# Kernel tuning notes

Hardware: AMD Instinct MI355X
Metric: run time of the kernel (lower is better)

## Reference

```python
import jax, jax.numpy as jnp
import numpy as np

H = 8          # nhead
EPS_Z = 1e-6   # linear-attention normalizer eps
LN_EPS = 1e-5  # torch LayerNorm default


def _ln(x, g, b):
    m = x.mean(-1, keepdims=True)
    v = ((x - m) ** 2).mean(-1, keepdims=True)
    return (x - m) * jax.lax.rsqrt(v + LN_EPS) * g + b


def setup_inputs() -> dict:
    key = jax.random.key(0)
    ks = jax.random.split(key, 8)
    B, S, E, F = 4, 8192, 512, 2048
    s = 0.02
    return {
        "src": jax.random.normal(ks[0], (B, S, E), jnp.float32),
        "Wq": jax.random.normal(ks[1], (E, E), jnp.float32) * s,
        "bq": jnp.zeros((E,), jnp.float32),
        "Wk": jax.random.normal(ks[2], (E, E), jnp.float32) * s,
        "bk": jnp.zeros((E,), jnp.float32),
        "Wv": jax.random.normal(ks[3], (E, E), jnp.float32) * s,
        "bv": jnp.zeros((E,), jnp.float32),
        "Wo": jax.random.normal(ks[4], (E, E), jnp.float32) * s,
        "bo": jnp.zeros((E,), jnp.float32),
        "W1": jax.random.normal(ks[5], (E, F), jnp.float32) * s,
        "b1": jnp.zeros((F,), jnp.float32),
        "W2": jax.random.normal(ks[6], (F, E), jnp.float32) * s,
        "b2": jnp.zeros((E,), jnp.float32),
        "g1": jnp.ones((E,), jnp.float32),
        "be1": jnp.zeros((E,), jnp.float32),
        "g2": jnp.ones((E,), jnp.float32),
        "be2": jnp.zeros((E,), jnp.float32),
    }


def reference(src, Wq, bq, Wk, bk, Wv, bv, Wo, bo, W1, b1, W2, b2, g1, be1, g2, be2):
    B, S, E = src.shape
    Dh = E // H

    def heads(x):  # [B,S,E] -> [B,H,S,Dh]
        return x.reshape(B, S, H, Dh).transpose(0, 2, 1, 3)

    q = heads(src @ Wq + bq)
    k = heads(src @ Wk + bk)
    v = heads(src @ Wv + bv)

    qm = jax.nn.elu(q) + 1.0  # feature map: ELU+1
    km = jax.nn.elu(k) + 1.0

    kv = jnp.einsum("bhsd,bhse->bhde", km, v)          # [B,H,Dh,Dh]
    ksum = km.sum(axis=2)                               # [B,H,Dh]
    z = 1.0 / (jnp.einsum("bhsd,bhd->bhs", qm, ksum) + EPS_Z)
    attn = jnp.einsum("bhsd,bhde->bhse", qm, kv) * z[..., None]

    attn = attn.transpose(0, 2, 1, 3).reshape(B, S, E) @ Wo + bo
    x = _ln(src + attn, g1, be1)
    ff = jax.nn.relu(x @ W1 + b1) @ W2 + b2
    return _ln(x + ff, g2, be2)
```

## Files before the change

kernel.cpp:

```cpp
#include <hip/hip_runtime.h>
#include <hip/hip_bf16.h>

typedef __attribute__((ext_vector_type(8))) short bf16x8;
typedef __attribute__((ext_vector_type(4))) float f32x4;

__device__ inline ushort f2bf(float f) {
    uint u = __float_as_uint(f);
    u += 0x7fff + ((u >> 16) & 1);
    return (ushort)(u >> 16);
}
__device__ inline float bf2f(ushort h) {
    return __uint_as_float(((uint)h) << 16);
}

__device__ inline void gload16(const void* g, void* lds) {
    __builtin_amdgcn_global_load_lds(
        (const __attribute__((address_space(1))) void*)g,
        (__attribute__((address_space(3))) void*)lds, 16, 0, 0);
}

__global__ void conv_bf16(const float* __restrict__ in, ushort* __restrict__ out, int n4) {
    int i = blockIdx.x * 256 + threadIdx.x;
    if (i >= n4) return;
    float4 a = ((const float4*)in)[i];
    ushort4 o;
    o.x = f2bf(a.x); o.y = f2bf(a.y); o.z = f2bf(a.z); o.w = f2bf(a.w);
    ((ushort4*)out)[i] = o;
}

__global__ void wconv_t(const float* __restrict__ in, ushort* __restrict__ out, int K, int N) {
    __shared__ float tile[32][33];
    int kb = blockIdx.y * 32, nb = blockIdx.x * 32;
    int tx = threadIdx.x & 31, ty = threadIdx.x >> 5;
#pragma unroll
    for (int i = 0; i < 4; i++)
        tile[ty + i * 8][tx] = in[(size_t)(kb + ty + i * 8) * N + nb + tx];
    __syncthreads();
#pragma unroll
    for (int i = 0; i < 4; i++) {
        int n = nb + ty + i * 8, k = kb + tx;
        out[(size_t)n * K + k] = f2bf(tile[tx][ty + i * 8]);
    }
}

__global__ void biascat(const float* __restrict__ a, const float* __restrict__ b,
                        const float* __restrict__ c, float* __restrict__ o) {
    int i = blockIdx.x * 256 + threadIdx.x;
    if (i < 512) o[i] = a[i];
    else if (i < 1024) o[i] = b[i - 512];
    else if (i < 1536) o[i] = c[i - 1024];
}

template <int EPI, int NT>
__global__ __launch_bounds__(512, 2) void gemm256(
    const ushort* __restrict__ A, const ushort* __restrict__ Bt,
    const float* __restrict__ bias, const ushort* __restrict__ res16,
    ushort* __restrict__ out16, int M, int N, int K, int nbxg) {
    extern __shared__ char smem[];
    const int t = threadIdx.x;
    const int w = t >> 6, l = t & 63;
    const int wr = w >> 2, wc = w & 3;
    const int nwg = gridDim.x;
    const int cpx = nwg >> 3;
    const int swz = (blockIdx.x & 7) * cpx + (blockIdx.x >> 3);
    const int bxg = swz % nbxg, by = swz / nbxg;
    const int bx0 = bxg * NT;

    const int sc = (t & 3) ^ ((t >> 3) & 3);
    const ushort* gA0 = A + (size_t)(by * 256 + (t >> 2)) * K + sc * 8;
    const ushort* gA1 = gA0 + (size_t)128 * K;
    const ushort* sB0 = Bt + (size_t)(bx0 * 256 + (t >> 2)) * K + sc * 8;
    const ushort* sB1 = sB0 + (size_t)128 * K;

    const int Kt = K >> 5;
    const int TOT = NT * Kt;
    int stg_kt = 0, stg_g = 0;

    auto stage_h0 = [&]() {
        char* Lb = smem + (stg_g & 3) * 32768 + (w << 10);
        gload16(gA0 + stg_kt * 32, Lb);
        gload16(sB0 + stg_kt * 32, Lb + 16384);
    };
    auto stage_h1 = [&]() {
        char* Lb = smem + (stg_g & 3) * 32768 + (w << 10);
        gload16(gA1 + stg_kt * 32, Lb + 8192);
        gload16(sB1 + stg_kt * 32, Lb + 24576);
        ++stg_g;
        if (++stg_kt == Kt) {
            stg_kt = 0;
            sB0 += (size_t)256 * K;
            sB1 += (size_t)256 * K;
        }
    };

    f32x4 acc[8][4] = {};

    const int R0a = wr * 128 + (l & 15);
    const int offA = R0a * 64 + (((l >> 4) ^ ((R0a >> 1) & 3)) << 4);
    const int R0b = wc * 64 + (l & 15);
    const int offB = 16384 + R0b * 64 + (((l >> 4) ^ ((R0b >> 1) & 3)) << 4);

    stage_h0(); stage_h1();
    stage_h0(); stage_h1();
    stage_h0(); stage_h1();

    int g = 0;
    for (int j = 0; j < NT; ++j) {
#pragma unroll 1
        for (int kt = 0; kt < Kt; ++kt, ++g) {
            const int rem = TOT - 1 - g;
            if (rem >= 2)      asm volatile("s_waitcnt vmcnt(8)" ::: "memory");
            else if (rem == 1) asm volatile("s_waitcnt vmcnt(4)" ::: "memory");
            else               asm volatile("s_waitcnt vmcnt(0)" ::: "memory");
            __builtin_amdgcn_s_barrier();
            __builtin_amdgcn_sched_barrier(0);

            const char* bufp = smem + (g & 3) * 32768;
            bf16x8 a[8], b[4];
            b[0] = *(const bf16x8*)(bufp + offB);
            b[1] = *(const bf16x8*)(bufp + offB + 1024);
            b[2] = *(const bf16x8*)(bufp + offB + 2048);
            b[3] = *(const bf16x8*)(bufp + offB + 3072);
            a[0] = *(const bf16x8*)(bufp + offA);
            a[1] = *(const bf16x8*)(bufp + offA + 1024);
            a[2] = *(const bf16x8*)(bufp + offA + 2048);
            a[3] = *(const bf16x8*)(bufp + offA + 3072);
            if (g + 3 < TOT) stage_h0();
            __builtin_amdgcn_sched_barrier(0);
            __builtin_amdgcn_s_barrier();
            asm volatile("s_waitcnt lgkmcnt(0)" ::: "memory");
            __builtin_amdgcn_sched_barrier(0);
            __builtin_amdgcn_s_setprio(1);
#pragma unroll
            for (int m = 0; m < 4; m++)
#pragma unroll
                for (int n = 0; n < 4; n++)
                    acc[m][n] = __builtin_amdgcn_mfma_f32_16x16x32_bf16(a[m], b[n], acc[m][n], 0, 0, 0);
            __builtin_amdgcn_s_setprio(0);
            __builtin_amdgcn_sched_barrier(0);
            a[4] = *(const bf16x8*)(bufp + offA + 4096);
            a[5] = *(const bf16x8*)(bufp + offA + 5120);
            a[6] = *(const bf16x8*)(bufp + offA + 6144);
            a[7] = *(const bf16x8*)(bufp + offA + 7168);
            if (g + 3 < TOT) stage_h1();
            __builtin_amdgcn_sched_barrier(0);
            __builtin_amdgcn_s_barrier();
            asm volatile("s_waitcnt lgkmcnt(0)" ::: "memory");
            __builtin_amdgcn_sched_barrier(0);
            __builtin_amdgcn_s_setprio(1);
#pragma unroll
            for (int m = 4; m < 8; m++)
#pragma unroll
                for (int n = 0; n < 4; n++)
                    acc[m][n] = __builtin_amdgcn_mfma_f32_16x16x32_bf16(a[m], b[n], acc[m][n], 0, 0, 0);
            __builtin_amdgcn_s_setprio(0);
            __builtin_amdgcn_sched_barrier(0);
        }

        {
            const int bx = bx0 + j;
            const int row0 = by * 256 + wr * 128 + ((l >> 4) << 2);
            const int col0 = bx * 256 + wc * 64 + (l & 15);
            const int seg = bx >> 1;
            const size_t segoff = (size_t)seg * M * 512;
            const int c511 = col0 & 511;
            float bv[4];
#pragma unroll
            for (int n = 0; n < 4; n++) bv[n] = bias[col0 + n * 16];
#pragma unroll
            for (int m = 0; m < 8; m++) {
#pragma unroll
                for (int r = 0; r < 4; r++) {
                    const int row = row0 + m * 16 + r;
                    const size_t base = (size_t)row * N + col0;
#pragma unroll
                    for (int n = 0; n < 4; n++) {
                        float vv = acc[m][n][r] + bv[n];
                        if constexpr (EPI == 2) {
                            vv = vv > 0.f ? vv : 0.f;
                            out16[base + n * 16] = f2bf(vv);
                        } else if constexpr (EPI == 3) {
                            vv += bf2f(res16[base + n * 16]);
                            out16[base + n * 16] = f2bf(vv);
                        } else if constexpr (EPI == 4) {
                            if (seg < 2) vv = vv > 0.f ? vv + 1.f : __expf(vv);
                            out16[segoff + (size_t)row * 512 + c511 + n * 16] = f2bf(vv);
                        } else {
                            out16[base + n * 16] = f2bf(vv);
                        }
                    }
                }
            }
            if (j + 1 < NT) {
#pragma unroll
                for (int m = 0; m < 8; m++)
#pragma unroll
                    for (int n = 0; n < 4; n++)
                        acc[m][n] = (f32x4){0.f, 0.f, 0.f, 0.f};
            }
        }
    }
}

__global__ __launch_bounds__(256) void kv_partial(
    const ushort* __restrict__ km, const ushort* __restrict__ v,
    float* __restrict__ kvp, float* __restrict__ ksump, int S) {
    __shared__ ushort kms[32 * 64];
    __shared__ ushort vs[32 * 64];
    const int t = threadIdx.x;
    const int bh = blockIdx.y, b = bh >> 3, h = bh & 7;
    const int d0 = (t >> 4) * 4, e0 = (t & 15) * 4;
    float acc[4][4] = {};
    float ks = 0.f;
    const int s_base = blockIdx.x * 512;
    const int r = t >> 3, c8 = (t & 7) * 8;
    for (int s0 = 0; s0 < 512; s0 += 32) {
        size_t grow = ((size_t)b * S + s_base + s0 + r) * 512 + h * 64 + c8;
        *(uint4*)&kms[r * 64 + c8] = *(const uint4*)&km[grow];
        *(uint4*)&vs[r * 64 + c8] = *(const uint4*)&v[grow];
        __syncthreads();
#pragma unroll 4
        for (int s = 0; s < 32; ++s) {
            ushort4 ka = *(const ushort4*)&kms[s * 64 + d0];
            ushort4 vb = *(const ushort4*)&vs[s * 64 + e0];
            float a0 = bf2f(ka.x), a1 = bf2f(ka.y), a2 = bf2f(ka.z), a3 = bf2f(ka.w);
            float b0 = bf2f(vb.x), b1 = bf2f(vb.y), b2 = bf2f(vb.z), b3 = bf2f(vb.w);
            acc[0][0] += a0 * b0; acc[0][1] += a0 * b1; acc[0][2] += a0 * b2; acc[0][3] += a0 * b3;
            acc[1][0] += a1 * b0; acc[1][1] += a1 * b1; acc[1][2] += a1 * b2; acc[1][3] += a1 * b3;
            acc[2][0] += a2 * b0; acc[2][1] += a2 * b1; acc[2][2] += a2 * b2; acc[2][3] += a2 * b3;
            acc[3][0] += a3 * b0; acc[3][1] += a3 * b1; acc[3][2] += a3 * b2; acc[3][3] += a3 * b3;
            if (t < 64) ks += bf2f(kms[s * 64 + t]);
        }
        __syncthreads();
    }
    float* dst = kvp + ((size_t)bh * 16 + blockIdx.x) * 4096;
#pragma unroll
    for (int i = 0; i < 4; i++)
#pragma unroll
        for (int j = 0; j < 4; j++)
            dst[(d0 + i) * 64 + e0 + j] = acc[i][j];
    if (t < 64) ksump[((size_t)bh * 16 + blockIdx.x) * 64 + t] = ks;
}

__global__ void kv_reduce(const float* __restrict__ kvp, const float* __restrict__ ksump,
                          ushort* __restrict__ kvt, float* __restrict__ ksum) {
    int i = blockIdx.x * 256 + threadIdx.x;
    if (i < 32 * 4096) {
        int bh = i >> 12, de = i & 4095;
        int d = de >> 6, e = de & 63;
        float s = 0.f;
#pragma unroll
        for (int c = 0; c < 16; ++c) s += kvp[((size_t)bh * 16 + c) * 4096 + de];
        kvt[(size_t)bh * 4096 + e * 64 + d] = f2bf(s);
    } else {
        int j = i - 32 * 4096;
        if (j < 32 * 64) {
            int bh = j >> 6, d = j & 63;
            float s = 0.f;
#pragma unroll
            for (int c = 0; c < 16; ++c) s += ksump[((size_t)bh * 16 + c) * 64 + d];
            ksum[j] = s;
        }
    }
}

__global__ __launch_bounds__(256) void attn_mfma(
    const ushort* __restrict__ qm, const ushort* __restrict__ kvt,
    const float* __restrict__ ksum, ushort* __restrict__ attnE, int S) {
    __shared__ ushort As[128 * 128];
    __shared__ ushort Bs[128 * 64];
    __shared__ float zbuf[128][2];
    __shared__ float ks2[128];
    const int t = threadIdx.x, w = t >> 6, l = t & 63;
    const int cx = blockIdx.x, by = blockIdx.y;
    const int b = (by * 128) / S;
    const int h0 = cx * 2;
    const size_t arow0 = (size_t)(by * 128) * 512 + cx * 128;

#pragma unroll
    for (int rd = 0; rd < 8; ++rd) {
        const ushort* g = qm + arow0 + (size_t)(rd * 16 + w * 4 + (l >> 4)) * 512 + (l & 15) * 8;
        gload16(g, (char*)As + rd * 4096 + w * 1024);
    }
    const ushort* kvbase = kvt + (size_t)(b * 8 + h0) * 4096;
#pragma unroll
    for (int rd = 0; rd < 4; ++rd) {
        const ushort* g = kvbase + (rd * 32 + w * 8 + (l >> 3)) * 64 + (l & 7) * 8;
        gload16(g, (char*)Bs + rd * 4096 + w * 1024);
    }
    if (t < 128) ks2[t] = ksum[(b * 8 + h0) * 64 + t];
    __syncthreads();

    {
        const int r = t >> 1, hh = t & 1;
        float den = 0.f;
#pragma unroll
        for (int d0 = 0; d0 < 64; d0 += 8) {
            bf16x8 qv = *(const bf16x8*)&As[r * 128 + hh * 64 + d0];
#pragma unroll
            for (int j = 0; j < 8; j++) den += bf2f((ushort)qv[j]) * ks2[hh * 64 + d0 + j];
        }
        zbuf[r][hh] = 1.0f / (den + 1e-6f);
    }

    const int wr = w >> 1, wc = w & 1;
    const int ar = wr * 64 + (l & 15);
    const int br = wc * 64 + (l & 15);
    const int ko = (l >> 4) * 8;
    f32x4 acc[4][4] = {};
#pragma unroll
    for (int ks_ = 0; ks_ < 2; ++ks_) {
        bf16x8 a[4], bb[4];
#pragma unroll
        for (int m = 0; m < 4; m++)
            a[m] = *(const bf16x8*)&As[(ar + m * 16) * 128 + wc * 64 + ks_ * 32 + ko];
#pragma unroll
        for (int n = 0; n < 4; n++)
            bb[n] = *(const bf16x8*)&Bs[(br + n * 16) * 64 + ks_ * 32 + ko];
#pragma unroll
        for (int m = 0; m < 4; m++)
#pragma unroll
            for (int n = 0; n < 4; n++)
                acc[m][n] = __builtin_amdgcn_mfma_f32_16x16x32_bf16(a[m], bb[n], acc[m][n], 0, 0, 0);
    }
    __syncthreads();

    const int row0l = wr * 64 + ((l >> 4) << 2);
    ushort* outbase = attnE + (size_t)(by * 128) * 512 + cx * 128;
#pragma unroll
    for (int n = 0; n < 4; n++) {
#pragma unroll
        for (int m = 0; m < 4; m++) {
#pragma unroll
            for (int r = 0; r < 4; r++) {
                int rl = row0l + m * 16 + r;
                float z = zbuf[rl][wc];
                outbase[(size_t)rl * 512 + wc * 64 + n * 16 + (l & 15)] = f2bf(acc[m][n][r] * z);
            }
        }
    }
}

template <int OUT32>
__global__ __launch_bounds__(256) void ln_bf16(
    const ushort* __restrict__ in, const float* __restrict__ g, const float* __restrict__ be,
    void* __restrict__ outp, int Mrows) {
    const int w = threadIdx.x >> 6, l = threadIdx.x & 63;
    const int row = blockIdx.x * 4 + w;
    if (row >= Mrows) return;
    const ushort* rp = in + (size_t)row * 512;
    uint4 u = *(const uint4*)&rp[l * 8];
    float x[8];
    x[0] = bf2f((ushort)(u.x & 0xffff)); x[1] = bf2f((ushort)(u.x >> 16));
    x[2] = bf2f((ushort)(u.y & 0xffff)); x[3] = bf2f((ushort)(u.y >> 16));
    x[4] = bf2f((ushort)(u.z & 0xffff)); x[5] = bf2f((ushort)(u.z >> 16));
    x[6] = bf2f((ushort)(u.w & 0xffff)); x[7] = bf2f((ushort)(u.w >> 16));
    float s = 0.f, ss = 0.f;
#pragma unroll
    for (int j = 0; j < 8; j++) { s += x[j]; ss += x[j] * x[j]; }
#pragma unroll
    for (int o = 1; o < 64; o <<= 1) {
        s += __shfl_xor(s, o, 64);
        ss += __shfl_xor(ss, o, 64);
    }
    float mean = s * (1.f / 512.f);
    float var = ss * (1.f / 512.f) - mean * mean;
    float rstd = rsqrtf(var + 1e-5f);
    float4 g0 = *(const float4*)&g[l * 8], g1v = *(const float4*)&g[l * 8 + 4];
    float4 b0 = *(const float4*)&be[l * 8], b1v = *(const float4*)&be[l * 8 + 4];
    float o0[8];
    o0[0] = (x[0] - mean) * rstd * g0.x + b0.x;
    o0[1] = (x[1] - mean) * rstd * g0.y + b0.y;
    o0[2] = (x[2] - mean) * rstd * g0.z + b0.z;
    o0[3] = (x[3] - mean) * rstd * g0.w + b0.w;
    o0[4] = (x[4] - mean) * rstd * g1v.x + b1v.x;
    o0[5] = (x[5] - mean) * rstd * g1v.y + b1v.y;
    o0[6] = (x[6] - mean) * rstd * g1v.z + b1v.z;
    o0[7] = (x[7] - mean) * rstd * g1v.w + b1v.w;
    if constexpr (OUT32) {
        float* op = (float*)outp + (size_t)row * 512;
        *(float4*)&op[l * 8] = make_float4(o0[0], o0[1], o0[2], o0[3]);
        *(float4*)&op[l * 8 + 4] = make_float4(o0[4], o0[5], o0[6], o0[7]);
    } else {
        ushort* op = (ushort*)outp + (size_t)row * 512;
        ushort4 u0, u1;
        u0.x = f2bf(o0[0]); u0.y = f2bf(o0[1]); u0.z = f2bf(o0[2]); u0.w = f2bf(o0[3]);
        u1.x = f2bf(o0[4]); u1.y = f2bf(o0[5]); u1.z = f2bf(o0[6]); u1.w = f2bf(o0[7]);
        *(ushort4*)&op[l * 8] = u0;
        *(ushort4*)&op[l * 8 + 4] = u1;
    }
}

extern "C" void kernel_launch(void* const* d_in, const int* in_sizes, int n_in,
                              void* d_out, int out_size, void* d_ws, size_t ws_size,
                              hipStream_t stream) {
    const int B = 4, S = 8192, E = 512, F = 2048;
    const int M = B * S;
    const size_t SZ = (size_t)M * E * 2;
    const int SMEM = 131072;

    const float* src = (const float*)d_in[0];
    const float* Wq = (const float*)d_in[1];  const float* bq = (const float*)d_in[2];
    const float* Wk = (const float*)d_in[3];  const float* bk = (const float*)d_in[4];
    const float* Wv = (const float*)d_in[5];  const float* bv = (const float*)d_in[6];
    const float* Wo = (const float*)d_in[7];  const float* bo = (const float*)d_in[8];
    const float* W1 = (const float*)d_in[9];  const float* b1 = (const float*)d_in[10];
    const float* W2 = (const float*)d_in[11]; const float* b2 = (const float*)d_in[12];
    const float* g1 = (const float*)d_in[13]; const float* be1 = (const float*)d_in[14];
    const float* g2 = (const float*)d_in[15]; const float* be2 = (const float*)d_in[16];

    char* ws = (char*)d_ws;
    ushort* qm    = (ushort*)(ws + 0 * SZ);
    ushort* km    = (ushort*)(ws + 1 * SZ);
    ushort* v     = (ushort*)(ws + 2 * SZ);
    ushort* src16 = (ushort*)(ws + 3 * SZ);
    ushort* x16   = (ushort*)(ws + 4 * SZ);
    ushort* z16   = (ushort*)(ws + 5 * SZ);
    char*   tail  = ws + 6 * SZ;
    float*  kvp   = (float*)(tail);
    float*  ksump = (float*)(tail + 8388608);
    ushort* kvt   = (ushort*)(tail + 8519680);
    float*  ksum  = (float*)(tail + 8781824);
    float*  bqkv  = (float*)(tail + 8790016);
    ushort* wqkv  = (ushort*)(tail + 8796160);
    ushort* wot   = (ushort*)(tail + 10369024);
    ushort* w1t   = (ushort*)(tail + 10893312);
    ushort* w2t   = (ushort*)(tail + 12990464);
    ushort* attnE = km;
    ushort* y16   = v;
    ushort* hbuf  = (ushort*)(ws + 0);

    hipFuncSetAttribute((const void*)gemm256<4, 3>, hipFuncAttributeMaxDynamicSharedMemorySize, SMEM);
    hipFuncSetAttribute((const void*)gemm256<3, 1>, hipFuncAttributeMaxDynamicSharedMemorySize, SMEM);
    hipFuncSetAttribute((const void*)gemm256<2, 4>, hipFuncAttributeMaxDynamicSharedMemorySize, SMEM);

    conv_bf16<<<dim3((M * E / 4 + 255) / 256), 256, 0, stream>>>(src, src16, M * E / 4);
    wconv_t<<<dim3(E / 32, E / 32), 256, 0, stream>>>(Wq, wqkv, E, E);
    wconv_t<<<dim3(E / 32, E / 32), 256, 0, stream>>>(Wk, wqkv + 512 * 512, E, E);
    wconv_t<<<dim3(E / 32, E / 32), 256, 0, stream>>>(Wv, wqkv + 1024 * 512, E, E);
    wconv_t<<<dim3(E / 32, E / 32), 256, 0, stream>>>(Wo, wot, E, E);
    wconv_t<<<dim3(F / 32, E / 32), 256, 0, stream>>>(W1, w1t, E, F);
    wconv_t<<<dim3(E / 32, F / 32), 256, 0, stream>>>(W2, w2t, F, E);
    biascat<<<dim3(6), 256, 0, stream>>>(bq, bk, bv, bqkv);

    gemm256<4, 3><<<dim3(2 * 128), 512, SMEM, stream>>>(src16, wqkv, bqkv, nullptr, qm, M, 1536, E, 2);

    kv_partial<<<dim3(16, 32), 256, 0, stream>>>(km, v, kvp, ksump, S);
    kv_reduce<<<dim3((32 * 4096 + 32 * 64 + 255) / 256), 256, 0, stream>>>(kvp, ksump, kvt, ksum);

    attn_mfma<<<dim3(4, M / 128), 256, 0, stream>>>(qm, kvt, ksum, attnE, S);

    gemm256<3, 1><<<dim3(2 * 128), 512, SMEM, stream>>>(attnE, wot, bo, src16, y16, M, E, E, 2);
    ln_bf16<0><<<dim3(M / 4), 256, 0, stream>>>(y16, g1, be1, x16, M);

    gemm256<2, 4><<<dim3(2 * 128), 512, SMEM, stream>>>(x16, w1t, b1, nullptr, hbuf, M, F, E, 2);
    gemm256<3, 1><<<dim3(2 * 128), 512, SMEM, stream>>>(hbuf, w2t, b2, x16, z16, M, E, F, 2);
    ln_bf16<1><<<dim3(M / 4), 256, 0, stream>>>(z16, g2, be2, (float*)d_out, M);
}
```

Before: 379.4 us.

## Fuse prep kernels, simplify GEMM stage loop, add M-grouped tiling for FFN1

Merges the bf16 conversion, weight transposes and bias concat into a single prep launch to cut launch overhead. The GEMM main loop now issues both global-to-LDS stage halves up front and does one LDS read phase followed by all 32 MFMAs, removing two inner barriers per k-step. A GB template flag lets FFN1 tiles walk along M for a fixed N column block (8x32 grid), so the W1 tile is reused across consecutive M blocks instead of the A tile. The restructured loop removes the interleaving of loads and MFMAs, which may expose more LDS latency.

```diff
diff --git a/kernel.cpp b/kernel.cpp
--- a/kernel.cpp
+++ b/kernel.cpp
@@ -19,43 +19,61 @@
         (__attribute__((address_space(3))) void*)lds, 16, 0, 0);
 }
 
-__global__ void conv_bf16(const float* __restrict__ in, ushort* __restrict__ out, int n4) {
-    int i = blockIdx.x * 256 + threadIdx.x;
-    if (i >= n4) return;
-    float4 a = ((const float4*)in)[i];
-    ushort4 o;
-    o.x = f2bf(a.x); o.y = f2bf(a.y); o.z = f2bf(a.z); o.w = f2bf(a.w);
-    ((ushort4*)out)[i] = o;
-}
-
-__global__ void wconv_t(const float* __restrict__ in, ushort* __restrict__ out, int K, int N) {
+__global__ __launch_bounds__(256) void prep(
+    const float* __restrict__ src, ushort* __restrict__ src16,
+    const float* __restrict__ Wq, const float* __restrict__ Wk,
+    const float* __restrict__ Wv, const float* __restrict__ Wo,
+    const float* __restrict__ W1, const float* __restrict__ W2,
+    ushort* __restrict__ wqkv, ushort* __restrict__ wot,
+    ushort* __restrict__ w1t, ushort* __restrict__ w2t,
+    const float* __restrict__ bq, const float* __restrict__ bk,
+    const float* __restrict__ bv, float* __restrict__ bqkv) {
     __shared__ float tile[32][33];
-    int kb = blockIdx.y * 32, nb = blockIdx.x * 32;
-    int tx = threadIdx.x & 31, ty = threadIdx.x >> 5;
+    int bid = blockIdx.x;
+    const int t = threadIdx.x;
+    if (bid < 16384) {
+        int i = bid * 256 + t;
+        float4 a = ((const float4*)src)[i];
+        ushort4 o;
+        o.x = f2bf(a.x); o.y = f2bf(a.y); o.z = f2bf(a.z); o.w = f2bf(a.w);
+        ((ushort4*)src16)[i] = o;
+        return;
+    }
+    bid -= 16384;
+    const float* in; ushort* out; int Kd, Nd;
+    if (bid < 1024) {
+        int m = bid >> 8;
+        in = (m == 0) ? Wq : (m == 1) ? Wk : (m == 2) ? Wv : Wo;
+        out = (m == 3) ? wot : (wqkv + m * 512 * 512);
+        Kd = 512; Nd = 512; bid &= 255;
+    } else if (bid < 2048) { in = W1; out = w1t; Kd = 512; Nd = 2048; bid -= 1024; }
+    else if (bid < 3072) { in = W2; out = w2t; Kd = 2048; Nd = 512; bid -= 2048; }
+    else {
+        int i = (bid - 3072) * 256 + t;
+        if (i < 512) bqkv[i] = bq[i];
+        else if (i < 1024) bqkv[i] = bk[i - 512];
+        else if (i < 1536) bqkv[i] = bv[i - 1024];
+        return;
+    }
+    const int nx = Nd / 32;
+    const int nbase = (bid % nx) * 32, kb = (bid / nx) * 32;
+    const int tx = t & 31, ty = t >> 5;
 #pragma unroll
     for (int i = 0; i < 4; i++)
-        tile[ty + i * 8][tx] = in[(size_t)(kb + ty + i * 8) * N + nb + tx];
+        tile[ty + i * 8][tx] = in[(size_t)(kb + ty + i * 8) * Nd + nbase + tx];
     __syncthreads();
 #pragma unroll
     for (int i = 0; i < 4; i++) {
-        int n = nb + ty + i * 8, k = kb + tx;
-        out[(size_t)n * K + k] = f2bf(tile[tx][ty + i * 8]);
-    }
-}
-
-__global__ void biascat(const float* __restrict__ a, const float* __restrict__ b,
-                        const float* __restrict__ c, float* __restrict__ o) {
-    int i = blockIdx.x * 256 + threadIdx.x;
-    if (i < 512) o[i] = a[i];
-    else if (i < 1024) o[i] = b[i - 512];
-    else if (i < 1536) o[i] = c[i - 1024];
-}
-
-template <int EPI, int NT>
+        int n = nbase + ty + i * 8, k = kb + tx;
+        out[(size_t)n * Kd + k] = f2bf(tile[tx][ty + i * 8]);
+    }
+}
+
+template <int EPI, int NT, int GB>
 __global__ __launch_bounds__(512, 2) void gemm256(
     const ushort* __restrict__ A, const ushort* __restrict__ Bt,
     const float* __restrict__ bias, const ushort* __restrict__ res16,
-    ushort* __restrict__ out16, int M, int N, int K, int nbxg) {
+    ushort* __restrict__ out16, int M, int N, int K, int nb1) {
     extern __shared__ char smem[];
     const int t = threadIdx.x;
     const int w = t >> 6, l = t & 63;
@@ -63,33 +81,35 @@
     const int nwg = gridDim.x;
     const int cpx = nwg >> 3;
     const int swz = (blockIdx.x & 7) * cpx + (blockIdx.x >> 3);
-    const int bxg = swz % nbxg, by = swz / nbxg;
-    const int bx0 = bxg * NT;
+    int bx0, by0;
+    if (GB == 0) { bx0 = (swz % nb1) * NT; by0 = swz / nb1; }
+    else         { bx0 = swz % nb1;        by0 = (swz / nb1) * NT; }
 
     const int sc = (t & 3) ^ ((t >> 3) & 3);
-    const ushort* gA0 = A + (size_t)(by * 256 + (t >> 2)) * K + sc * 8;
+    const ushort* gA0 = A + (size_t)(by0 * 256 + (t >> 2)) * K + sc * 8;
     const ushort* gA1 = gA0 + (size_t)128 * K;
-    const ushort* sB0 = Bt + (size_t)(bx0 * 256 + (t >> 2)) * K + sc * 8;
-    const ushort* sB1 = sB0 + (size_t)128 * K;
+    const ushort* gB0 = Bt + (size_t)(bx0 * 256 + (t >> 2)) * K + sc * 8;
+    const ushort* gB1 = gB0 + (size_t)128 * K;
 
     const int Kt = K >> 5;
     const int TOT = NT * Kt;
     int stg_kt = 0, stg_g = 0;
+    size_t stgA = 0, stgB = 0;
 
     auto stage_h0 = [&]() {
         char* Lb = smem + (stg_g & 3) * 32768 + (w << 10);
-        gload16(gA0 + stg_kt * 32, Lb);
-        gload16(sB0 + stg_kt * 32, Lb + 16384);
+        gload16(gA0 + stgA + stg_kt * 32, Lb);
+        gload16(gB0 + stgB + stg_kt * 32, Lb + 16384);
     };
     auto stage_h1 = [&]() {
         char* Lb = smem + (stg_g & 3) * 32768 + (w << 10);
-        gload16(gA1 + stg_kt * 32, Lb + 8192);
-        gload16(sB1 + stg_kt * 32, Lb + 24576);
+        gload16(gA1 + stgA + stg_kt * 32, Lb + 8192);
+        gload16(gB1 + stgB + stg_kt * 32, Lb + 24576);
         ++stg_g;
         if (++stg_kt == Kt) {
             stg_kt = 0;
-            sB0 += (size_t)256 * K;
-            sB1 += (size_t)256 * K;
+            if (GB == 0) stgB += (size_t)256 * K;
+            else         stgA += (size_t)256 * K;
         }
     };
 
@@ -116,49 +136,27 @@
             __builtin_amdgcn_sched_barrier(0);
 
             const char* bufp = smem + (g & 3) * 32768;
+            if (g + 3 < TOT) { stage_h0(); stage_h1(); }
+
             bf16x8 a[8], b[4];
-            b[0] = *(const bf16x8*)(bufp + offB);
-            b[1] = *(const bf16x8*)(bufp + offB + 1024);
-            b[2] = *(const bf16x8*)(bufp + offB + 2048);
-            b[3] = *(const bf16x8*)(bufp + offB + 3072);
-            a[0] = *(const bf16x8*)(bufp + offA);
-            a[1] = *(const bf16x8*)(bufp + offA + 1024);
-            a[2] = *(const bf16x8*)(bufp + offA + 2048);
-            a[3] = *(const bf16x8*)(bufp + offA + 3072);
-            if (g + 3 < TOT) stage_h0();
-            __builtin_amdgcn_sched_barrier(0);
-            __builtin_amdgcn_s_barrier();
-            asm volatile("s_waitcnt lgkmcnt(0)" ::: "memory");
-            __builtin_amdgcn_sched_barrier(0);
+#pragma unroll
+            for (int n = 0; n < 4; n++) b[n] = *(const bf16x8*)(bufp + offB + n * 1024);
+#pragma unroll
+            for (int m = 0; m < 8; m++) a[m] = *(const bf16x8*)(bufp + offA + m * 1024);
+
             __builtin_amdgcn_s_setprio(1);
 #pragma unroll
-            for (int m = 0; m < 4; m++)
+            for (int m = 0; m < 8; m++)
 #pragma unroll
                 for (int n = 0; n < 4; n++)
                     acc[m][n] = __builtin_amdgcn_mfma_f32_16x16x32_bf16(a[m], b[n], acc[m][n], 0, 0, 0);
             __builtin_amdgcn_s_setprio(0);
             __builtin_amdgcn_sched_barrier(0);
-            a[4] = *(const bf16x8*)(bufp + offA + 4096);
-            a[5] = *(const bf16x8*)(bufp + offA + 5120);
-            a[6] = *(const bf16x8*)(bufp + offA + 6144);
-            a[7] = *(const bf16x8*)(bufp + offA + 7168);
-            if (g + 3 < TOT) stage_h1();
-            __builtin_amdgcn_sched_barrier(0);
-            __builtin_amdgcn_s_barrier();
-            asm volatile("s_waitcnt lgkmcnt(0)" ::: "memory");
-            __builtin_amdgcn_sched_barrier(0);
-            __builtin_amdgcn_s_setprio(1);
-#pragma unroll
-            for (int m = 4; m < 8; m++)
-#pragma unroll
-                for (int n = 0; n < 4; n++)
-                    acc[m][n] = __builtin_amdgcn_mfma_f32_16x16x32_bf16(a[m], b[n], acc[m][n], 0, 0, 0);
-            __builtin_amdgcn_s_setprio(0);
-            __builtin_amdgcn_sched_barrier(0);
         }
 
         {
-            const int bx = bx0 + j;
+            const int bx = (GB == 0) ? (bx0 + j) : bx0;
+            const int by = (GB == 0) ? by0 : (by0 + j);
             const int row0 = by * 256 + wr * 128 + ((l >> 4) << 2);
             const int col0 = bx * 256 + wc * 64 + (l & 15);
             const int seg = bx >> 1;
@@ -430,30 +428,24 @@
     ushort* y16   = v;
     ushort* hbuf  = (ushort*)(ws + 0);
 
-    hipFuncSetAttribute((const void*)gemm256<4, 3>, hipFuncAttributeMaxDynamicSharedMemorySize, SMEM);
-    hipFuncSetAttribute((const void*)gemm256<3, 1>, hipFuncAttributeMaxDynamicSharedMemorySize, SMEM);
-    hipFuncSetAttribute((const void*)gemm256<2, 4>, hipFuncAttributeMaxDynamicSharedMemorySize, SMEM);
-
-    conv_bf16<<<dim3((M * E / 4 + 255) / 256), 256, 0, stream>>>(src, src16, M * E / 4);
-    wconv_t<<<dim3(E / 32, E / 32), 256, 0, stream>>>(Wq, wqkv, E, E);
-    wconv_t<<<dim3(E / 32, E / 32), 256, 0, stream>>>(Wk, wqkv + 512 * 512, E, E);
-    wconv_t<<<dim3(E / 32, E / 32), 256, 0, stream>>>(Wv, wqkv + 1024 * 512, E, E);
-    wconv_t<<<dim3(E / 32, E / 32), 256, 0, stream>>>(Wo, wot, E, E);
-    wconv_t<<<dim3(F / 32, E / 32), 256, 0, stream>>>(W1, w1t, E, F);
-    wconv_t<<<dim3(E / 32, F / 32), 256, 0, stream>>>(W2, w2t, F, E);
-    biascat<<<dim3(6), 256, 0, stream>>>(bq, bk, bv, bqkv);
-
-    gemm256<4, 3><<<dim3(2 * 128), 512, SMEM, stream>>>(src16, wqkv, bqkv, nullptr, qm, M, 1536, E, 2);
+    hipFuncSetAttribute((const void*)gemm256<4, 3, 0>, hipFuncAttributeMaxDynamicSharedMemorySize, SMEM);
+    hipFuncSetAttribute((const void*)gemm256<3, 1, 0>, hipFuncAttributeMaxDynamicSharedMemorySize, SMEM);
+    hipFuncSetAttribute((const void*)gemm256<2, 4, 1>, hipFuncAttributeMaxDynamicSharedMemorySize, SMEM);
+
+    prep<<<dim3(16384 + 3072 + 6), 256, 0, stream>>>(
+        src, src16, Wq, Wk, Wv, Wo, W1, W2, wqkv, wot, w1t, w2t, bq, bk, bv, bqkv);
+
+    gemm256<4, 3, 0><<<dim3(2 * 128), 512, SMEM, stream>>>(src16, wqkv, bqkv, nullptr, qm, M, 1536, E, 2);
 
     kv_partial<<<dim3(16, 32), 256, 0, stream>>>(km, v, kvp, ksump, S);
     kv_reduce<<<dim3((32 * 4096 + 32 * 64 + 255) / 256), 256, 0, stream>>>(kvp, ksump, kvt, ksum);
 
     attn_mfma<<<dim3(4, M / 128), 256, 0, stream>>>(qm, kvt, ksum, attnE, S);
 
-    gemm256<3, 1><<<dim3(2 * 128), 512, SMEM, stream>>>(attnE, wot, bo, src16, y16, M, E, E, 2);
+    gemm256<3, 1, 0><<<dim3(2 * 128), 512, SMEM, stream>>>(attnE, wot, bo, src16, y16, M, E, E, 2);
     ln_bf16<0><<<dim3(M / 4), 256, 0, stream>>>(y16, g1, be1, x16, M);
 
-    gemm256<2, 4><<<dim3(2 * 128), 512, SMEM, stream>>>(x16, w1t, b1, nullptr, hbuf, M, F, E, 2);
-    gemm256<3, 1><<<dim3(2 * 128), 512, SMEM, stream>>>(hbuf, w2t, b2, x16, z16, M, E, F, 2);
+    gemm256<2, 4, 1><<<dim3(8 * 32), 512, SMEM, stream>>>(x16, w1t, b1, nullptr, hbuf, M, F, E, 8);
+    gemm256<3, 1, 0><<<dim3(2 * 128), 512, SMEM, stream>>>(hbuf, w2t, b2, x16, z16, M, E, F, 2);
     ln_bf16<1><<<dim3(M / 4), 256, 0, stream>>>(z16, g2, be2, (float*)d_out, M);
 }
```

New measurement: 364.8 us. 3.8% less time.
